# Kernel tuning notes

Measured on AMD Instinct MI355X. Metric: run time of the kernel, lower is better.

The kernel has to match this reference:

```python
import jax, jax.numpy as jnp
import numpy as np

HIDDEN = 768


def _rotary(x):
    # x: [B, S, H]; matches torch sinusoidal_position_embedding + rotary math
    B, S, H = x.shape
    pos = jnp.arange(S, dtype=jnp.float32)[:, None]            # [S, 1]
    inv_freq = jnp.power(10000.0, -2.0 * jnp.arange(H // 2, dtype=jnp.float32) / H)
    ang = pos * inv_freq                                       # [S, H/2]
    cos = jnp.repeat(jnp.cos(ang), 2, axis=-1)                 # cos_pos = pos_emb[...,1::2] repeated
    sin = jnp.repeat(jnp.sin(ang), 2, axis=-1)                 # sin_pos = pos_emb[...,::2] repeated
    x_rot = jnp.stack([-x[..., 1::2], x[..., ::2]], axis=-1).reshape(x.shape)
    return x * cos + x_rot * sin


def setup_inputs() -> dict:
    key = jax.random.key(0)
    k1, k2, k3, k4 = jax.random.split(key, 4)
    B, N, M, H = 4, 128, 128, HIDDEN
    review = jax.random.normal(k1, (B, N, H), dtype=jnp.float32)
    reply = jax.random.normal(k2, (B, M, H), dtype=jnp.float32)
    # nn.Linear(2H, H): weight [H, 2H], bias [H]
    bound = 1.0 / np.sqrt(2 * H)
    W = jax.random.uniform(k3, (H, 2 * H), dtype=jnp.float32, minval=-bound, maxval=bound)
    b = jax.random.uniform(k4, (H,), dtype=jnp.float32, minval=-bound, maxval=bound)
    return {"review": review, "reply": reply, "W": W, "b": b}


def reference(review, reply, W, b):
    # rotary position embedding on both inputs
    review = _rotary(review)   # [B, N, H]
    reply = _rotary(reply)     # [B, M, H]
    H = review.shape[-1]
    # Linear on concat([review, reply]) == review @ W_r^T + reply @ W_p^T + b
    W_r, W_p = W[:, :H], W[:, H:]                         # each [H, H]
    proj_review = jnp.einsum('bnh,oh->bno', review, W_r)  # [B, N, H]
    proj_reply = jnp.einsum('bmh,oh->bmo', reply, W_p)    # [B, M, H]
    out = proj_review[:, :, None, :] + proj_reply[:, None, :, :] + b  # [B, N, M, H]
    return jax.nn.relu(out)
```

## Files before the change

kernel.cpp:

```cpp
#include <hip/hip_runtime.h>

#define HID   768
#define BATCH 4
#define SEQ   128
#define NROWS 512
#define PAIRS_PER_MAT (NROWS * (HID/2))

typedef __bf16 bf16x8 __attribute__((ext_vector_type(8)));
typedef float  floatx4 __attribute__((ext_vector_type(4)));

__device__ __forceinline__ unsigned short f2bf(float x) {
    unsigned u = __builtin_bit_cast(unsigned, x);
    unsigned r = u + 0x7FFFu + ((u >> 16) & 1u);
    return (unsigned short)(r >> 16);
}

__global__ __launch_bounds__(256) void rotary_kernel(
    const float* __restrict__ review,
    const float* __restrict__ reply,
    unsigned short* __restrict__ rot)
{
    int p   = blockIdx.x * 256 + threadIdx.x;
    int mat = (p >= PAIRS_PER_MAT) ? 1 : 0;
    int rem = p - mat * PAIRS_PER_MAT;
    int row = rem / (HID / 2);
    int i   = rem - row * (HID / 2);
    int s   = row & 127;

    const float* src = (mat ? reply : review) + row * HID + 2 * i;
    float2 x = *reinterpret_cast<const float2*>(src);

    float inv = exp2f(-(float)i * (13.287712379549449f / 384.0f));
    float ang = (float)s * inv;
    float c  = cosf(ang);
    float sn = sinf(ang);

    float oe = x.x * c - x.y * sn;
    float oo = x.y * c + x.x * sn;
    unsigned pk = (unsigned)f2bf(oe) | ((unsigned)f2bf(oo) << 16);
    *reinterpret_cast<unsigned*>(rot + (size_t)mat * (NROWS * HID) + row * HID + 2 * i) = pk;
}

__global__ __launch_bounds__(256) void gemm_kernel(
    const unsigned short* __restrict__ rot,
    const float* __restrict__ W,
    float* __restrict__ proj)
{
    __shared__ __align__(16) unsigned short As[64 * 32];
    __shared__ __align__(16) unsigned short Bs[64 * 32];

    const int tid  = threadIdx.x;
    const int lane = tid & 63;
    const int wave = tid >> 6;
    const int mat  = blockIdx.z;
    const int row0 = blockIdx.y * 64;
    const int col0 = blockIdx.x * 64;
    const int q    = lane >> 4;
    const int r16  = lane & 15;

    const unsigned short* Abase = rot + (size_t)mat * (NROWS * HID);
    const int srow  = tid >> 2;
    const int skoff = (tid & 3) * 8;

    floatx4 acc[4];
#pragma unroll
    for (int c = 0; c < 4; ++c) acc[c] = (floatx4)0.0f;

    for (int k0 = 0; k0 < HID; k0 += 32) {
        __syncthreads();
        *reinterpret_cast<uint4*>(&As[srow * 32 + skoff]) =
            *reinterpret_cast<const uint4*>(&Abase[(row0 + srow) * HID + k0 + skoff]);
        {
            const float* wp = W + (size_t)(col0 + srow) * (2 * HID) + mat * HID + k0 + skoff;
            float4 w0 = *reinterpret_cast<const float4*>(wp);
            float4 w1 = *reinterpret_cast<const float4*>(wp + 4);
            uint4 pk;
            pk.x = (unsigned)f2bf(w0.x) | ((unsigned)f2bf(w0.y) << 16);
            pk.y = (unsigned)f2bf(w0.z) | ((unsigned)f2bf(w0.w) << 16);
            pk.z = (unsigned)f2bf(w1.x) | ((unsigned)f2bf(w1.y) << 16);
            pk.w = (unsigned)f2bf(w1.z) | ((unsigned)f2bf(w1.w) << 16);
            *reinterpret_cast<uint4*>(&Bs[srow * 32 + skoff]) = pk;
        }
        __syncthreads();

        bf16x8 af = *reinterpret_cast<const bf16x8*>(&As[(wave * 16 + r16) * 32 + q * 8]);
#pragma unroll
        for (int c = 0; c < 4; ++c) {
            bf16x8 bf = *reinterpret_cast<const bf16x8*>(&Bs[(c * 16 + r16) * 32 + q * 8]);
            acc[c] = __builtin_amdgcn_mfma_f32_16x16x32_bf16(af, bf, acc[c], 0, 0, 0);
        }
    }

    float* pbase = proj + (size_t)mat * (NROWS * HID);
#pragma unroll
    for (int c = 0; c < 4; ++c) {
        int col = col0 + c * 16 + r16;
#pragma unroll
        for (int rg = 0; rg < 4; ++rg) {
            int row = row0 + wave * 16 + q * 4 + rg;
            pbase[row * HID + col] = acc[c][rg];
        }
    }
}

__global__ __launch_bounds__(256) void bcast_kernel(
    const float* __restrict__ proj,
    const float* __restrict__ bias,
    float* __restrict__ out)
{
    const int bn    = blockIdx.x;
    const int chunk = blockIdx.y;
    const int b     = bn >> 7;

    __shared__ __align__(16) float prb[HID];
    const float* pr  = proj + (size_t)bn * HID;
    const float* ppb = proj + (size_t)(NROWS + b * SEQ + chunk * 16) * HID;
    for (int o = threadIdx.x; o < HID; o += 256)
        prb[o] = pr[o] + bias[o];
    __syncthreads();

    float* obase = out + (size_t)bn * (SEQ * HID) + (size_t)chunk * 16 * HID;
#pragma unroll 4
    for (int it = 0; it < 12; ++it) {
        int idx = it * 256 + threadIdx.x;
        int m   = idx / 192;
        int t   = idx - m * 192;
        int o4  = t * 4;

        floatx4 p = *reinterpret_cast<const floatx4*>(ppb + m * HID + o4);
        floatx4 a = *reinterpret_cast<const floatx4*>(&prb[o4]);
        floatx4 r;
        r.x = fmaxf(a.x + p.x, 0.0f);
        r.y = fmaxf(a.y + p.y, 0.0f);
        r.z = fmaxf(a.z + p.z, 0.0f);
        r.w = fmaxf(a.w + p.w, 0.0f);
        __builtin_nontemporal_store(r, reinterpret_cast<floatx4*>(obase + m * HID + o4));
    }
}

extern "C" void kernel_launch(void* const* d_in, const int* in_sizes, int n_in,
                              void* d_out, int out_size, void* d_ws, size_t ws_size,
                              hipStream_t stream) {
    const float* review = (const float*)d_in[0];
    const float* reply  = (const float*)d_in[1];
    const float* W      = (const float*)d_in[2];
    const float* bias   = (const float*)d_in[3];
    float* out = (float*)d_out;

    unsigned short* rot = (unsigned short*)d_ws;
    float* proj = (float*)((char*)d_ws + (size_t)2 * NROWS * HID * sizeof(unsigned short));

    rotary_kernel<<<PAIRS_PER_MAT * 2 / 256, 256, 0, stream>>>(review, reply, rot);
    dim3 g2(HID / 64, NROWS / 64, 2);
    gemm_kernel<<<g2, 256, 0, stream>>>(rot, W, proj);
    dim3 g3(NROWS, 8);
    bcast_kernel<<<g3, 256, 0, stream>>>(proj, bias, out);
}
```

Baseline: 244.6 us.

## Prefetch larger K chunks in GEMM, use fast sincos, drop nontemporal stores

The GEMM now stages 192-wide K chunks (padded row stride of 200) in shared memory. The next chunk is prefetched into registers while MFMAs run on the current one, which cuts the number of barriers and hides global load latency. The rotary kernel switches to the fast __sincosf intrinsic, which can lose accuracy at large angles. The broadcast kernel's nontemporal stores become plain stores, which changes cache behaviour on the dominant 200MB output write.

```diff
diff --git a/kernel.cpp b/kernel.cpp
--- a/kernel.cpp
+++ b/kernel.cpp
@@ -1,7 +1,6 @@
 #include <hip/hip_runtime.h>
 
 #define HID   768
-#define BATCH 4
 #define SEQ   128
 #define NROWS 512
 #define PAIRS_PER_MAT (NROWS * (HID/2))
@@ -30,10 +29,9 @@
     const float* src = (mat ? reply : review) + row * HID + 2 * i;
     float2 x = *reinterpret_cast<const float2*>(src);
 
-    float inv = exp2f(-(float)i * (13.287712379549449f / 384.0f));
-    float ang = (float)s * inv;
-    float c  = cosf(ang);
-    float sn = sinf(ang);
+    float inv = exp2f((float)i * (-13.287712379549449f / 384.0f));
+    float sn, c;
+    __sincosf((float)s * inv, &sn, &c);
 
     float oe = x.x * c - x.y * sn;
     float oo = x.y * c + x.x * sn;
@@ -46,8 +44,8 @@
     const float* __restrict__ W,
     float* __restrict__ proj)
 {
-    __shared__ __align__(16) unsigned short As[64 * 32];
-    __shared__ __align__(16) unsigned short Bs[64 * 32];
+    __shared__ __align__(16) unsigned short As[64 * 200];
+    __shared__ __align__(16) unsigned short Bs[64 * 200];
 
     const int tid  = threadIdx.x;
     const int lane = tid & 63;
@@ -58,37 +56,59 @@
     const int q    = lane >> 4;
     const int r16  = lane & 15;
 
-    const unsigned short* Abase = rot + (size_t)mat * (NROWS * HID);
-    const int srow  = tid >> 2;
-    const int skoff = (tid & 3) * 8;
+    const int srow = tid >> 2;
+    const int sko  = (tid & 3) * 48;
+
+    const unsigned short* Arow = rot + (size_t)mat * (NROWS * HID)
+                                     + (size_t)(row0 + srow) * HID + sko;
+    const float* Wrow = W + (size_t)(col0 + srow) * (2 * HID) + mat * HID + sko;
 
     floatx4 acc[4];
 #pragma unroll
     for (int c = 0; c < 4; ++c) acc[c] = (floatx4)0.0f;
 
-    for (int k0 = 0; k0 < HID; k0 += 32) {
-        __syncthreads();
-        *reinterpret_cast<uint4*>(&As[srow * 32 + skoff]) =
-            *reinterpret_cast<const uint4*>(&Abase[(row0 + srow) * HID + k0 + skoff]);
-        {
-            const float* wp = W + (size_t)(col0 + srow) * (2 * HID) + mat * HID + k0 + skoff;
-            float4 w0 = *reinterpret_cast<const float4*>(wp);
-            float4 w1 = *reinterpret_cast<const float4*>(wp + 4);
+    uint4   aR[6];
+    floatx4 wR[12];
+#pragma unroll
+    for (int j = 0; j < 6; ++j)  aR[j] = *reinterpret_cast<const uint4*>(Arow + j * 8);
+#pragma unroll
+    for (int j = 0; j < 12; ++j) wR[j] = *reinterpret_cast<const floatx4*>(Wrow + j * 4);
+
+    for (int ch = 0; ch < 4; ++ch) {
+#pragma unroll
+        for (int j = 0; j < 6; ++j)
+            *reinterpret_cast<uint4*>(&As[srow * 200 + sko + j * 8]) = aR[j];
+#pragma unroll
+        for (int j = 0; j < 6; ++j) {
+            floatx4 w0 = wR[2 * j], w1 = wR[2 * j + 1];
             uint4 pk;
             pk.x = (unsigned)f2bf(w0.x) | ((unsigned)f2bf(w0.y) << 16);
             pk.y = (unsigned)f2bf(w0.z) | ((unsigned)f2bf(w0.w) << 16);
             pk.z = (unsigned)f2bf(w1.x) | ((unsigned)f2bf(w1.y) << 16);
             pk.w = (unsigned)f2bf(w1.z) | ((unsigned)f2bf(w1.w) << 16);
-            *reinterpret_cast<uint4*>(&Bs[srow * 32 + skoff]) = pk;
+            *reinterpret_cast<uint4*>(&Bs[srow * 200 + sko + j * 8]) = pk;
         }
         __syncthreads();
 
-        bf16x8 af = *reinterpret_cast<const bf16x8*>(&As[(wave * 16 + r16) * 32 + q * 8]);
+        if (ch < 3) {
 #pragma unroll
-        for (int c = 0; c < 4; ++c) {
-            bf16x8 bf = *reinterpret_cast<const bf16x8*>(&Bs[(c * 16 + r16) * 32 + q * 8]);
-            acc[c] = __builtin_amdgcn_mfma_f32_16x16x32_bf16(af, bf, acc[c], 0, 0, 0);
+            for (int j = 0; j < 6; ++j)
+                aR[j] = *reinterpret_cast<const uint4*>(Arow + (ch + 1) * 192 + j * 8);
+#pragma unroll
+            for (int j = 0; j < 12; ++j)
+                wR[j] = *reinterpret_cast<const floatx4*>(Wrow + (ch + 1) * 192 + j * 4);
         }
+
+#pragma unroll
+        for (int kk = 0; kk < 6; ++kk) {
+            bf16x8 af = *reinterpret_cast<const bf16x8*>(&As[(wave * 16 + r16) * 200 + kk * 32 + q * 8]);
+#pragma unroll
+            for (int c = 0; c < 4; ++c) {
+                bf16x8 bf = *reinterpret_cast<const bf16x8*>(&Bs[(c * 16 + r16) * 200 + kk * 32 + q * 8]);
+                acc[c] = __builtin_amdgcn_mfma_f32_16x16x32_bf16(af, bf, acc[c], 0, 0, 0);
+            }
+        }
+        __syncthreads();
     }
 
     float* pbase = proj + (size_t)mat * (NROWS * HID);
@@ -134,7 +154,7 @@
         r.y = fmaxf(a.y + p.y, 0.0f);
         r.z = fmaxf(a.z + p.z, 0.0f);
         r.w = fmaxf(a.w + p.w, 0.0f);
-        __builtin_nontemporal_store(r, reinterpret_cast<floatx4*>(obase + m * HID + o4));
+        *reinterpret_cast<floatx4*>(obase + m * HID + o4) = r;
     }
 }
 
@@ -148,7 +168,7 @@
     float* out = (float*)d_out;
 
     unsigned short* rot = (unsigned short*)d_ws;
-    float* proj = (float*)((char*)d_ws + (size_t)2 * NROWS * HID * sizeof(unsigned short));
+    float* proj = (float*)((char*)d_ws + (size_t)2 * NROWS * HID * 2);
 
     rotary_kernel<<<PAIRS_PER_MAT * 2 / 256, 256, 0, stream>>>(review, reply, rot);
     dim3 g2(HID / 64, NROWS / 64, 2);
```

Result: faster. 225.4 us (-7.8%).
